# Optimization experiments

Measured on AMD Instinct MI355X. Metric: run time of the kernel, lower is better.

Reference implementation:

```python
import jax, jax.numpy as jnp
import numpy as np

B, N, S, C1, C2 = 8, 8192, 2048, 128, 256
H1, H2 = 256, 256
EPS_LN = 1e-5


def _layernorm_c(x, g, b):
    # LayerNorm over channel dim of [B, C, N]
    mu = jnp.mean(x, axis=1, keepdims=True)
    var = jnp.mean((x - mu) ** 2, axis=1, keepdims=True)
    return g[None, :, None] * (x - mu) / jnp.sqrt(var + EPS_LN) + b[None, :, None]


def setup_inputs() -> dict:
    key = jax.random.key(0)
    ks = jax.random.split(key, 8)
    Cin = C1 + C2
    return {
        "points_coor1": jax.random.normal(ks[0], (B, 3, N), jnp.float32),
        "points_coor2": jax.random.normal(ks[1], (B, 3, S), jnp.float32),
        "points_fea1": jax.random.normal(ks[2], (B, C1, N), jnp.float32),
        "points_fea2": jax.random.normal(ks[3], (B, C2, S), jnp.float32),
        "points_padding2": jnp.zeros((B, S), dtype=bool),
        "W1": jax.random.normal(ks[4], (H1, Cin), jnp.float32) * 0.05,
        "b1": jnp.zeros((H1,), jnp.float32),
        "g1": jnp.ones((H1,), jnp.float32),
        "be1": jnp.zeros((H1,), jnp.float32),
        "W2": jax.random.normal(ks[5], (H2, H1), jnp.float32) * 0.05,
        "b2": jnp.zeros((H2,), jnp.float32),
        "g2": jnp.ones((H2,), jnp.float32),
        "be2": jnp.zeros((H2,), jnp.float32),
    }


def reference(points_coor1, points_coor2, points_fea1, points_fea2,
              points_padding2, W1, b1, g1, be1, W2, b2, g2, be2):
    c1 = jnp.transpose(points_coor1, (0, 2, 1))  # [B,N,3]
    c2 = jnp.transpose(points_coor2, (0, 2, 1))  # [B,S,3]
    f2 = jnp.transpose(points_fea2, (0, 2, 1))   # [B,S,C2]

    # push padded points far away (max computed on unmodified coords, as in torch RHS-first eval)
    big = jnp.max(jnp.abs(c2)) * 3.0
    c2 = jnp.where(points_padding2[..., None], big, c2)

    # squared euclidean pairwise distances [B,N,S]
    d = (jnp.sum(c1 * c1, -1)[:, :, None]
         + jnp.sum(c2 * c2, -1)[:, None, :]
         - 2.0 * jnp.einsum('bnd,bsd->bns', c1, c2))

    neg_d, idx = jax.lax.top_k(-d, 3)          # 3 smallest distances
    dists = -neg_d                              # [B,N,3]
    recip = 1.0 / jnp.clip(dists, 1e-8)
    w = recip / jnp.sum(recip, axis=-1, keepdims=True)  # [B,N,3]

    gathered = jax.vmap(lambda f, i: f[i])(f2, idx)     # [B,N,3,C2]
    interp = jnp.einsum('bnkc,bnk->bcn', gathered, w)   # [B,C2,N]

    x = jnp.concatenate([points_fea1, interp], axis=1)  # [B,C1+C2,N]
    x = jax.nn.relu(_layernorm_c(jnp.einsum('oc,bcn->bon', W1, x) + b1[None, :, None], g1, be1))
    x = jax.nn.relu(_layernorm_c(jnp.einsum('oc,bcn->bon', W2, x) + b2[None, :, None], g2, be2))
    return x
```

## Files before the change

kernel.cpp:

```cpp
#include <hip/hip_runtime.h>
#include <stdint.h>

#define BB 8
#define NPT 8192
#define SPT 2048
#define C1D 128
#define C2D 256
#define CIN 384
#define HD 256
#define SPLIT 8
#define SC (SPT/SPLIT)

typedef __attribute__((ext_vector_type(8))) short bf16x8;
typedef __attribute__((ext_vector_type(4))) float f32x4;

__device__ __forceinline__ unsigned short f2b(float f){
  unsigned int u = __float_as_uint(f);
  u += 0x7fffu + ((u >> 16) & 1u);
  return (unsigned short)(u >> 16);
}

__device__ __forceinline__ void bar_sync(){
  __builtin_amdgcn_sched_barrier(0);
  asm volatile("s_waitcnt lgkmcnt(0)" ::: "memory");
  __builtin_amdgcn_s_barrier();
  __builtin_amdgcn_sched_barrier(0);
}

__global__ __launch_bounds__(256) void cvt2_bf16_kernel(const float* __restrict__ W1,
    const float* __restrict__ W2, unsigned short* __restrict__ dst){
  int i = blockIdx.x * 256 + threadIdx.x;
  const int n1 = HD * CIN;
  if (i < n1) dst[i] = f2b(W1[i]);
  else {
    int k = i - n1;
    if (k < HD * HD) dst[n1 + k] = f2b(W2[k]);
  }
}

__global__ __launch_bounds__(256) void gsrc_kernel(const float* __restrict__ coor2,
    const unsigned char* __restrict__ pad, float4* __restrict__ gs){
  int i = blockIdx.x * 256 + threadIdx.x;
  int b = i >> 11, s = i & (SPT - 1);
  const float* cb = coor2 + b * 3 * SPT;
  float x = cb[s], y = cb[SPT + s], z = cb[2*SPT + s];
  if (pad[i]) { x = 1e19f; y = 1e19f; z = 1e19f; }
  float n2 = __fadd_rn(__fadd_rn(__fmul_rn(x,x), __fmul_rn(y,y)), __fmul_rn(z,z));
  gs[i] = make_float4(x, y, z, n2);
}

__global__ __launch_bounds__(256) void transpose_cn(const float* __restrict__ src,
    unsigned short* __restrict__ dst, int Cdim, int Ndim, int dstStride){
  __shared__ unsigned short t[32][33];
  int b = blockIdx.z;
  int n0 = blockIdx.x * 32, c0 = blockIdx.y * 32;
  int tx = threadIdx.x, ty = threadIdx.y;
  const float* s = src + (size_t)b * Cdim * Ndim;
  unsigned short* d = dst + (size_t)b * Ndim * dstStride;
  #pragma unroll
  for (int i = 0; i < 4; i++)
    t[ty + i*8][tx] = f2b(s[(size_t)(c0 + ty + i*8) * Ndim + n0 + tx]);
  __syncthreads();
  #pragma unroll
  for (int i = 0; i < 4; i++)
    d[(size_t)(n0 + ty + i*8) * dstStride + c0 + tx] = t[tx][ty + i*8];
}

__global__ __launch_bounds__(256) void knn_part_kernel(const float* __restrict__ coor1,
    const float4* __restrict__ gs, float* __restrict__ cv, int* __restrict__ cj){
  int b = blockIdx.y, c = blockIdx.z;
  int s0c = c * SC;
  const float4* gsb = gs + b * SPT + s0c;
  int n = blockIdx.x * 256 + threadIdx.x;
  const float* ca = coor1 + b * 3 * NPT;
  float x1 = ca[n], y1 = ca[NPT + n], z1 = ca[2*NPT + n];
  float n1 = __fadd_rn(__fadd_rn(__fmul_rn(x1,x1), __fmul_rn(y1,y1)), __fmul_rn(z1,z1));
  float v0 = 3.4e38f, v1 = 3.4e38f, v2 = 3.4e38f;
  int j0 = 0, j1 = 0, j2 = 0;
  #pragma unroll 8
  for (int s = 0; s < SC; s++){
    float4 q = gsb[s];
    float dot = __fadd_rn(__fadd_rn(__fmul_rn(x1,q.x), __fmul_rn(y1,q.y)), __fmul_rn(z1,q.z));
    float npn = __fadd_rn(n1, q.w);
    float d = __builtin_fmaf(-2.0f, dot, npn);
    bool l0 = d < v0, l1 = d < v1, l2 = d < v2;
    j2 = l1 ? j1 : (l2 ? s : j2);
    j1 = l0 ? j0 : (l1 ? s : j1);
    j0 = l0 ? s  : j0;
    float nv2 = __builtin_amdgcn_fmed3f(v1, v2, d);
    float nv1 = __builtin_amdgcn_fmed3f(v0, v1, d);
    v0 = fminf(v0, d); v1 = nv1; v2 = nv2;
  }
  size_t m = (size_t)b * NPT + n;
  size_t base = (m * SPLIT + c) * 3;
  cv[base+0] = v0; cv[base+1] = v1; cv[base+2] = v2;
  cj[base+0] = s0c + j0; cj[base+1] = s0c + j1; cj[base+2] = s0c + j2;
}

__global__ __launch_bounds__(256) void knn_merge_kernel(const float* __restrict__ cv,
    const int* __restrict__ cj, float* __restrict__ w3, int* __restrict__ i3){
  size_t m = (size_t)blockIdx.x * 256 + threadIdx.x;
  float v0 = 3.4e38f, v1 = 3.4e38f, v2 = 3.4e38f;
  int j0 = 0, j1 = 0, j2 = 0;
  #pragma unroll
  for (int c = 0; c < SPLIT; c++){
    #pragma unroll
    for (int k = 0; k < 3; k++){
      float d = cv[(m * SPLIT + c) * 3 + k];
      int j   = cj[(m * SPLIT + c) * 3 + k];
      bool l0 = d < v0, l1 = d < v1, l2 = d < v2;
      j2 = l1 ? j1 : (l2 ? j : j2);
      j1 = l0 ? j0 : (l1 ? j : j1);
      j0 = l0 ? j  : j0;
      float nv2 = __builtin_amdgcn_fmed3f(v1, v2, d);
      float nv1 = __builtin_amdgcn_fmed3f(v0, v1, d);
      v0 = fminf(v0, d); v1 = nv1; v2 = nv2;
    }
  }
  float r0 = 1.0f / fmaxf(v0, 1e-8f);
  float r1 = 1.0f / fmaxf(v1, 1e-8f);
  float r2 = 1.0f / fmaxf(v2, 1e-8f);
  float rs = (r0 + r1) + r2;
  w3[m*3+0] = r0 / rs; w3[m*3+1] = r1 / rs; w3[m*3+2] = r2 / rs;
  i3[m*3+0] = j0; i3[m*3+1] = j1; i3[m*3+2] = j2;
}

__global__ __launch_bounds__(256) void interp_kernel(const unsigned short* __restrict__ f2t,
    const float* __restrict__ w3, const int* __restrict__ i3, unsigned short* __restrict__ xpm){
  int m = blockIdx.x * 4 + (threadIdx.x >> 6);
  int lane = threadIdx.x & 63;
  int b = m >> 13;
  int s0 = i3[m*3+0], s1 = i3[m*3+1], s2 = i3[m*3+2];
  float w0 = w3[m*3+0], w1 = w3[m*3+1], w2 = w3[m*3+2];
  const ushort4 a = *(const ushort4*)(f2t + (size_t)(b*SPT + s0) * C2D + lane*4);
  const ushort4 c = *(const ushort4*)(f2t + (size_t)(b*SPT + s1) * C2D + lane*4);
  const ushort4 e = *(const ushort4*)(f2t + (size_t)(b*SPT + s2) * C2D + lane*4);
  #define B2F(u) __uint_as_float(((unsigned int)(u)) << 16)
  ushort4 o;
  o.x = f2b(w0*B2F(a.x) + w1*B2F(c.x) + w2*B2F(e.x));
  o.y = f2b(w0*B2F(a.y) + w1*B2F(c.y) + w2*B2F(e.y));
  o.z = f2b(w0*B2F(a.z) + w1*B2F(c.z) + w2*B2F(e.z));
  o.w = f2b(w0*B2F(a.w) + w1*B2F(c.w) + w2*B2F(e.w));
  *(ushort4*)(xpm + (size_t)m * CIN + C1D + lane*4) = o;
}

__global__ __launch_bounds__(256) void mlp_fused_kernel(const unsigned short* __restrict__ xpm,
    const unsigned short* __restrict__ W1g, const unsigned short* __restrict__ W2g,
    const float* __restrict__ b1, const float* __restrict__ g1, const float* __restrict__ be1,
    const float* __restrict__ b2, const float* __restrict__ g2, const float* __restrict__ be2,
    float* __restrict__ outg){
  __shared__ __align__(16) unsigned short Ws[256*40];
  __shared__ __align__(16) unsigned short Hbuf[64*264];
  __shared__ float sB[256], sG[256], sBe[256];
  unsigned short* Xs = Hbuf;
  int tid = threadIdx.x;
  int m0 = blockIdx.x * 64;
  int b = m0 >> 13, n0 = m0 & (NPT - 1);
  sB[tid] = b1[tid]; sG[tid] = g1[tid]; sBe[tid] = be1[tid];
  int w = tid >> 6, lane = tid & 63, col = lane & 15, quad = lane >> 4;
  int ml = w*16 + col;
  int mr = tid >> 2, part = tid & 3;
  const int4* wsrc  = (const int4*)(W1g + (size_t)tid * CIN);
  const int4* xsrc  = (const int4*)(xpm + (size_t)(m0 + mr) * CIN + part*8);
  f32x4 acc[16];
  #pragma unroll
  for (int i = 0; i < 16; i++) acc[i] = (f32x4)0.0f;

  int4 wA0 = wsrc[0], wA1 = wsrc[1], wA2 = wsrc[2], wA3 = wsrc[3];
  int4 xA  = xsrc[0];
  for (int c = 0; c < 12; c++){
    bar_sync();
    {
      int4* d4 = (int4*)(Ws + tid * 40);
      d4[0] = wA0; d4[1] = wA1; d4[2] = wA2; d4[3] = wA3;
      *(int4*)(Xs + mr*40 + part*8) = xA;
    }
    if (c + 1 < 12){
      wA0 = wsrc[(c+1)*4 + 0]; wA1 = wsrc[(c+1)*4 + 1];
      wA2 = wsrc[(c+1)*4 + 2]; wA3 = wsrc[(c+1)*4 + 3];
      xA  = xsrc[(c+1)*4];
    }
    bar_sync();
    bf16x8 bfrag = *(const bf16x8*)(Xs + ml*40 + quad*8);
    #pragma unroll
    for (int ot = 0; ot < 16; ot++){
      bf16x8 afrag = *(const bf16x8*)(Ws + (ot*16 + col)*40 + quad*8);
      acc[ot] = __builtin_amdgcn_mfma_f32_16x16x32_bf16(afrag, bfrag, acc[ot], 0, 0, 0);
    }
  }
  const int4* w2src = (const int4*)(W2g + (size_t)tid * HD);
  int4 v0r = w2src[0], v1r = w2src[1], v2r = w2src[2], v3r = w2src[3];
  float rb2 = b2[tid], rg2 = g2[tid], rbe2 = be2[tid];
  {
    float s1 = 0.f, s2 = 0.f;
    #pragma unroll
    for (int ot = 0; ot < 16; ot++)
      #pragma unroll
      for (int r = 0; r < 4; r++){
        int o = ot*16 + quad*4 + r;
        float v = acc[ot][r] + sB[o];
        acc[ot][r] = v;
        s1 += v; s2 += v*v;
      }
    s1 += __shfl_xor(s1, 16); s1 += __shfl_xor(s1, 32);
    s2 += __shfl_xor(s2, 16); s2 += __shfl_xor(s2, 32);
    float mu = s1 * (1.f/256.f);
    float rinv = rsqrtf(s2 * (1.f/256.f) - mu*mu + 1e-5f);
    bar_sync();
    #pragma unroll
    for (int ot = 0; ot < 16; ot++){
      int ob = ot*16 + quad*4;
      ushort4 hv;
      hv.x = f2b(fmaxf((acc[ot][0] - mu) * rinv * sG[ob+0] + sBe[ob+0], 0.f));
      hv.y = f2b(fmaxf((acc[ot][1] - mu) * rinv * sG[ob+1] + sBe[ob+1], 0.f));
      hv.z = f2b(fmaxf((acc[ot][2] - mu) * rinv * sG[ob+2] + sBe[ob+2], 0.f));
      hv.w = f2b(fmaxf((acc[ot][3] - mu) * rinv * sG[ob+3] + sBe[ob+3], 0.f));
      *(ushort4*)(Hbuf + ml*264 + ot*16 + quad*4) = hv;
    }
  }
  bar_sync();
  sB[tid] = rb2; sG[tid] = rg2; sBe[tid] = rbe2;

  #pragma unroll
  for (int i = 0; i < 16; i++) acc[i] = (f32x4)0.0f;
  for (int c = 0; c < 8; c++){
    bar_sync();
    {
      int4* d4 = (int4*)(Ws + tid * 40);
      d4[0] = v0r; d4[1] = v1r; d4[2] = v2r; d4[3] = v3r;
    }
    if (c + 1 < 8){
      v0r = w2src[(c+1)*4 + 0]; v1r = w2src[(c+1)*4 + 1];
      v2r = w2src[(c+1)*4 + 2]; v3r = w2src[(c+1)*4 + 3];
    }
    bar_sync();
    bf16x8 bfrag = *(const bf16x8*)(Hbuf + ml*264 + c*32 + quad*8);
    #pragma unroll
    for (int ot = 0; ot < 16; ot++){
      bf16x8 afrag = *(const bf16x8*)(Ws + (ot*16 + col)*40 + quad*8);
      acc[ot] = __builtin_amdgcn_mfma_f32_16x16x32_bf16(afrag, bfrag, acc[ot], 0, 0, 0);
    }
  }
  float s1 = 0.f, s2 = 0.f;
  #pragma unroll
  for (int ot = 0; ot < 16; ot++)
    #pragma unroll
    for (int r = 0; r < 4; r++){
      int o = ot*16 + quad*4 + r;
      float v = acc[ot][r] + sB[o];
      acc[ot][r] = v;
      s1 += v; s2 += v*v;
    }
  s1 += __shfl_xor(s1, 16); s1 += __shfl_xor(s1, 32);
  s2 += __shfl_xor(s2, 16); s2 += __shfl_xor(s2, 32);
  float mu = s1 * (1.f/256.f);
  float rinv = rsqrtf(s2 * (1.f/256.f) - mu*mu + 1e-5f);
  size_t obase = (size_t)b * HD * NPT + n0 + w*16 + col;
  #pragma unroll
  for (int ot = 0; ot < 16; ot++)
    #pragma unroll
    for (int r = 0; r < 4; r++){
      int o = ot*16 + quad*4 + r;
      float v = (acc[ot][r] - mu) * rinv * sG[o] + sBe[o];
      outg[obase + (size_t)o * NPT] = fmaxf(v, 0.f);
    }
}

extern "C" void kernel_launch(void* const* d_in, const int* in_sizes, int n_in,
                              void* d_out, int out_size, void* d_ws, size_t ws_size,
                              hipStream_t stream){
  const float* coor1 = (const float*)d_in[0];
  const float* coor2 = (const float*)d_in[1];
  const float* fea1  = (const float*)d_in[2];
  const float* fea2  = (const float*)d_in[3];
  const unsigned char* pad = (const unsigned char*)d_in[4];
  const float* W1  = (const float*)d_in[5];
  const float* b1  = (const float*)d_in[6];
  const float* g1  = (const float*)d_in[7];
  const float* be1 = (const float*)d_in[8];
  const float* W2  = (const float*)d_in[9];
  const float* b2  = (const float*)d_in[10];
  const float* g2  = (const float*)d_in[11];
  const float* be2 = (const float*)d_in[12];
  float* out = (float*)d_out;

  char* ws = (char*)d_ws;
  float* w3            = (float*)(ws + 256);
  int*   i3            = (int*)  (ws + 786688);
  unsigned short* W1b  = (unsigned short*)(ws + 1573120);
  unsigned short* W2b  = (unsigned short*)(ws + 1769728);
  unsigned short* f2t  = (unsigned short*)(ws + 1900800);
  unsigned short* xpm  = (unsigned short*)(ws + 10289408);
  float* cv            = (float*)(ws + 60621056);
  int*   cj            = (int*)  (ws + 60621056 + 6291456);
  float4* gs           = (float4*)(ws + 60621056 + 16777216);

  cvt2_bf16_kernel<<<(HD*CIN + HD*HD + 255)/256, 256, 0, stream>>>(W1, W2, W1b);
  gsrc_kernel<<<BB*SPT/256, 256, 0, stream>>>(coor2, pad, gs);
  dim3 tb(32, 8);
  transpose_cn<<<dim3(SPT/32, C2D/32, BB), tb, 0, stream>>>(fea2, f2t, C2D, SPT, C2D);
  transpose_cn<<<dim3(NPT/32, C1D/32, BB), tb, 0, stream>>>(fea1, xpm, C1D, NPT, CIN);
  knn_part_kernel<<<dim3(NPT/256, BB, SPLIT), 256, 0, stream>>>(coor1, gs, cv, cj);
  knn_merge_kernel<<<BB*NPT/256, 256, 0, stream>>>(cv, cj, w3, i3);
  interp_kernel<<<BB*NPT/4, 256, 0, stream>>>(f2t, w3, i3, xpm);
  mlp_fused_kernel<<<BB*NPT/64, 256, 0, stream>>>(xpm, W1b, W2b, b1, g1, be1, b2, g2, be2, out);
}
```

Measured before the change: 256.8 us.

## Merge prep kernels into one launch and fuse KNN merge into interpolation

Four preprocessing kernels (weight bf16 conversion, source-point packing, two transposes) become one launch that picks its task from the block index. The KNN merge step moves into the interpolation kernel, so the w3/i3 intermediate buffers and one launch go away. The cost is that each of the 64 lanes handling a point now reads and merges all 24 candidates on its own, repeating that work across lanes.

After: 271.6 us. 5.8% more time.

```diff
diff --git a/kernel.cpp b/kernel.cpp
--- a/kernel.cpp
+++ b/kernel.cpp
@@ -27,34 +27,46 @@
   __builtin_amdgcn_sched_barrier(0);
 }
 
-__global__ __launch_bounds__(256) void cvt2_bf16_kernel(const float* __restrict__ W1,
-    const float* __restrict__ W2, unsigned short* __restrict__ dst){
-  int i = blockIdx.x * 256 + threadIdx.x;
-  const int n1 = HD * CIN;
-  if (i < n1) dst[i] = f2b(W1[i]);
-  else {
-    int k = i - n1;
-    if (k < HD * HD) dst[n1 + k] = f2b(W2[k]);
-  }
-}
-
-__global__ __launch_bounds__(256) void gsrc_kernel(const float* __restrict__ coor2,
-    const unsigned char* __restrict__ pad, float4* __restrict__ gs){
-  int i = blockIdx.x * 256 + threadIdx.x;
-  int b = i >> 11, s = i & (SPT - 1);
-  const float* cb = coor2 + b * 3 * SPT;
-  float x = cb[s], y = cb[SPT + s], z = cb[2*SPT + s];
-  if (pad[i]) { x = 1e19f; y = 1e19f; z = 1e19f; }
-  float n2 = __fadd_rn(__fadd_rn(__fmul_rn(x,x), __fmul_rn(y,y)), __fmul_rn(z,z));
-  gs[i] = make_float4(x, y, z, n2);
-}
-
-__global__ __launch_bounds__(256) void transpose_cn(const float* __restrict__ src,
-    unsigned short* __restrict__ dst, int Cdim, int Ndim, int dstStride){
+#define NB_CVT 640
+#define NB_GSRC 64
+#define NB_T2 4096
+#define NB_T1 8192
+__global__ __launch_bounds__(256) void prep_kernel(
+    const float* __restrict__ W1, const float* __restrict__ W2, unsigned short* __restrict__ Wb,
+    const float* __restrict__ coor2, const unsigned char* __restrict__ pad, float4* __restrict__ gs,
+    const float* __restrict__ fea2, unsigned short* __restrict__ f2t,
+    const float* __restrict__ fea1, unsigned short* __restrict__ xpm){
   __shared__ unsigned short t[32][33];
-  int b = blockIdx.z;
-  int n0 = blockIdx.x * 32, c0 = blockIdx.y * 32;
-  int tx = threadIdx.x, ty = threadIdx.y;
+  int bid = blockIdx.x, tid = threadIdx.x;
+  if (bid < NB_CVT){
+    int i = bid * 256 + tid;
+    const int n1 = HD * CIN;
+    if (i < n1) Wb[i] = f2b(W1[i]);
+    else { int k = i - n1; if (k < HD * HD) Wb[n1 + k] = f2b(W2[k]); }
+    return;
+  }
+  bid -= NB_CVT;
+  if (bid < NB_GSRC){
+    int i = bid * 256 + tid;
+    int b = i >> 11, s = i & (SPT - 1);
+    const float* cb = coor2 + b * 3 * SPT;
+    float x = cb[s], y = cb[SPT + s], z = cb[2*SPT + s];
+    if (pad[i]) { x = 1e19f; y = 1e19f; z = 1e19f; }
+    float n2 = __fadd_rn(__fadd_rn(__fmul_rn(x,x), __fmul_rn(y,y)), __fmul_rn(z,z));
+    gs[i] = make_float4(x, y, z, n2);
+    return;
+  }
+  bid -= NB_GSRC;
+  const float* src; unsigned short* dst; int Cdim, Ndim, dstStride, n0, c0, b;
+  if (bid < NB_T2){
+    src = fea2; dst = f2t; Cdim = C2D; Ndim = SPT; dstStride = C2D;
+    n0 = (bid & 63) * 32; c0 = ((bid >> 6) & 7) * 32; b = bid >> 9;
+  } else {
+    bid -= NB_T2;
+    src = fea1; dst = xpm; Cdim = C1D; Ndim = NPT; dstStride = CIN;
+    n0 = (bid & 255) * 32; c0 = ((bid >> 8) & 3) * 32; b = bid >> 10;
+  }
+  int tx = tid & 31, ty = tid >> 5;
   const float* s = src + (size_t)b * Cdim * Ndim;
   unsigned short* d = dst + (size_t)b * Ndim * dstStride;
   #pragma unroll
@@ -97,17 +109,20 @@
   cj[base+0] = s0c + j0; cj[base+1] = s0c + j1; cj[base+2] = s0c + j2;
 }
 
-__global__ __launch_bounds__(256) void knn_merge_kernel(const float* __restrict__ cv,
-    const int* __restrict__ cj, float* __restrict__ w3, int* __restrict__ i3){
-  size_t m = (size_t)blockIdx.x * 256 + threadIdx.x;
+__global__ __launch_bounds__(256) void interp_kernel(const float* __restrict__ cv,
+    const int* __restrict__ cj, const unsigned short* __restrict__ f2t,
+    unsigned short* __restrict__ xpm){
+  int m = blockIdx.x * 4 + (threadIdx.x >> 6);
+  int lane = threadIdx.x & 63;
+  int b = m >> 13;
   float v0 = 3.4e38f, v1 = 3.4e38f, v2 = 3.4e38f;
   int j0 = 0, j1 = 0, j2 = 0;
   #pragma unroll
   for (int c = 0; c < SPLIT; c++){
     #pragma unroll
     for (int k = 0; k < 3; k++){
-      float d = cv[(m * SPLIT + c) * 3 + k];
-      int j   = cj[(m * SPLIT + c) * 3 + k];
+      float d = cv[((size_t)m * SPLIT + c) * 3 + k];
+      int j   = cj[((size_t)m * SPLIT + c) * 3 + k];
       bool l0 = d < v0, l1 = d < v1, l2 = d < v2;
       j2 = l1 ? j1 : (l2 ? j : j2);
       j1 = l0 ? j0 : (l1 ? j : j1);
@@ -121,20 +136,10 @@
   float r1 = 1.0f / fmaxf(v1, 1e-8f);
   float r2 = 1.0f / fmaxf(v2, 1e-8f);
   float rs = (r0 + r1) + r2;
-  w3[m*3+0] = r0 / rs; w3[m*3+1] = r1 / rs; w3[m*3+2] = r2 / rs;
-  i3[m*3+0] = j0; i3[m*3+1] = j1; i3[m*3+2] = j2;
-}
-
-__global__ __launch_bounds__(256) void interp_kernel(const unsigned short* __restrict__ f2t,
-    const float* __restrict__ w3, const int* __restrict__ i3, unsigned short* __restrict__ xpm){
-  int m = blockIdx.x * 4 + (threadIdx.x >> 6);
-  int lane = threadIdx.x & 63;
-  int b = m >> 13;
-  int s0 = i3[m*3+0], s1 = i3[m*3+1], s2 = i3[m*3+2];
-  float w0 = w3[m*3+0], w1 = w3[m*3+1], w2 = w3[m*3+2];
-  const ushort4 a = *(const ushort4*)(f2t + (size_t)(b*SPT + s0) * C2D + lane*4);
-  const ushort4 c = *(const ushort4*)(f2t + (size_t)(b*SPT + s1) * C2D + lane*4);
-  const ushort4 e = *(const ushort4*)(f2t + (size_t)(b*SPT + s2) * C2D + lane*4);
+  float w0 = r0 / rs, w1 = r1 / rs, w2 = r2 / rs;
+  const ushort4 a = *(const ushort4*)(f2t + (size_t)(b*SPT + j0) * C2D + lane*4);
+  const ushort4 c = *(const ushort4*)(f2t + (size_t)(b*SPT + j1) * C2D + lane*4);
+  const ushort4 e = *(const ushort4*)(f2t + (size_t)(b*SPT + j2) * C2D + lane*4);
   #define B2F(u) __uint_as_float(((unsigned int)(u)) << 16)
   ushort4 o;
   o.x = f2b(w0*B2F(a.x) + w1*B2F(c.x) + w2*B2F(e.x));
@@ -285,23 +290,16 @@
   float* out = (float*)d_out;
 
   char* ws = (char*)d_ws;
-  float* w3            = (float*)(ws + 256);
-  int*   i3            = (int*)  (ws + 786688);
   unsigned short* W1b  = (unsigned short*)(ws + 1573120);
-  unsigned short* W2b  = (unsigned short*)(ws + 1769728);
   unsigned short* f2t  = (unsigned short*)(ws + 1900800);
   unsigned short* xpm  = (unsigned short*)(ws + 10289408);
   float* cv            = (float*)(ws + 60621056);
   int*   cj            = (int*)  (ws + 60621056 + 6291456);
   float4* gs           = (float4*)(ws + 60621056 + 16777216);
 
-  cvt2_bf16_kernel<<<(HD*CIN + HD*HD + 255)/256, 256, 0, stream>>>(W1, W2, W1b);
-  gsrc_kernel<<<BB*SPT/256, 256, 0, stream>>>(coor2, pad, gs);
-  dim3 tb(32, 8);
-  transpose_cn<<<dim3(SPT/32, C2D/32, BB), tb, 0, stream>>>(fea2, f2t, C2D, SPT, C2D);
-  transpose_cn<<<dim3(NPT/32, C1D/32, BB), tb, 0, stream>>>(fea1, xpm, C1D, NPT, CIN);
+  prep_kernel<<<NB_CVT + NB_GSRC + NB_T2 + NB_T1, 256, 0, stream>>>(
+      W1, W2, W1b, coor2, pad, gs, fea2, f2t, fea1, xpm);
   knn_part_kernel<<<dim3(NPT/256, BB, SPLIT), 256, 0, stream>>>(coor1, gs, cv, cj);
-  knn_merge_kernel<<<BB*NPT/256, 256, 0, stream>>>(cv, cj, w3, i3);
-  interp_kernel<<<BB*NPT/4, 256, 0, stream>>>(f2t, w3, i3, xpm);
-  mlp_fused_kernel<<<BB*NPT/64, 256, 0, stream>>>(xpm, W1b, W2b, b1, g1, be1, b2, g2, be2, out);
-}
+  interp_kernel<<<BB*NPT/4, 256, 0, stream>>>(cv, cj, f2t, xpm);
+  mlp_fused_kernel<<<BB*NPT/64, 256, 0, stream>>>(xpm, W1b, W1b + HD*CIN, b1, g1, be1, b2, g2, be2, out);
+}
```
